# Performance work log

Hardware: AMD Instinct MI355X
Metric: run time of the kernel (lower is better)

Reference implementation:

```python
import jax, jax.numpy as jnp
import numpy as np

CHANNELS = 512
COND_DIM = 768
NUM_HEADS = 8
NUM_GROUPS = 32
EPS = 1e-5


def setup_inputs() -> dict:
    key = jax.random.key(0)
    ks = jax.random.split(key, 8)
    B, H, W, C, S = 8, 64, 64, CHANNELS, 256
    x = jax.random.normal(ks[0], (B, H, W, C), dtype=jnp.float32)
    cond_tokens = jax.random.normal(ks[1], (B, S, COND_DIM), dtype=jnp.float32)
    gn_scale = jnp.ones((C,), dtype=jnp.float32)
    gn_bias = jnp.zeros((C,), dtype=jnp.float32)
    Wq = jax.random.normal(ks[2], (C, CHANNELS), dtype=jnp.float32) * 0.02
    Wk = jax.random.normal(ks[3], (COND_DIM, CHANNELS), dtype=jnp.float32) * 0.02
    Wv = jax.random.normal(ks[4], (COND_DIM, CHANNELS), dtype=jnp.float32) * 0.02
    Wo = jax.random.normal(ks[5], (CHANNELS, CHANNELS), dtype=jnp.float32) * 0.02
    bo = jnp.zeros((CHANNELS,), dtype=jnp.float32)
    return {"x": x, "cond_tokens": cond_tokens, "gn_scale": gn_scale,
            "gn_bias": gn_bias, "Wq": Wq, "Wk": Wk, "Wv": Wv, "Wo": Wo, "bo": bo}


def group_norm(x, scale, bias):
    # x: (B,H,W,C); normalize over H,W and channels within each of NUM_GROUPS groups
    b, h, w, c = x.shape
    xg = x.reshape(b, h, w, NUM_GROUPS, c // NUM_GROUPS)
    mean = jnp.mean(xg, axis=(1, 2, 4), keepdims=True)
    var = jnp.var(xg, axis=(1, 2, 4), keepdims=True)
    xn = (xg - mean) * jax.lax.rsqrt(var + EPS)
    return xn.reshape(b, h, w, c) * scale + bias


def reference(x, cond_tokens, gn_scale, gn_bias, Wq, Wk, Wv, Wo, bo):
    b, h, w, c = x.shape
    head_dim = CHANNELS // NUM_HEADS
    x_seq = group_norm(x, gn_scale, gn_bias).reshape(b, h * w, c)
    # projections
    q = (x_seq @ Wq).reshape(b, -1, NUM_HEADS, head_dim).transpose(0, 2, 1, 3)
    k = (cond_tokens @ Wk).reshape(b, -1, NUM_HEADS, head_dim).transpose(0, 2, 1, 3)
    v = (cond_tokens @ Wv).reshape(b, -1, NUM_HEADS, head_dim).transpose(0, 2, 1, 3)
    scores = jnp.einsum('bhqd,bhkd->bhqk', q, k) / np.sqrt(head_dim).astype(np.float32)
    attn = jax.nn.softmax(scores, axis=-1)
    out = jnp.einsum('bhqk,bhkd->bhqd', attn, v)
    out = out.transpose(0, 2, 1, 3).reshape(b, h * w, CHANNELS)
    out = out @ Wo + bo
    return x + out.reshape(b, h, w, c)
```

## Files before the change

### kernel.cpp

```cpp
#include <hip/hip_runtime.h>
#include <hip/hip_bf16.h>

typedef unsigned short u16;
typedef unsigned int u32;
typedef __attribute__((ext_vector_type(8))) __bf16 bf16x8;
typedef __attribute__((ext_vector_type(4))) float f32x4;
typedef __attribute__((ext_vector_type(16))) float f32x16;
typedef __attribute__((ext_vector_type(4))) u32 u32x4;

#define DEVFN static __device__ __forceinline__

DEVFN float bf2f(u16 v) { union { u32 u; float f; } x; x.u = (u32)v << 16; return x.f; }
DEVFN u16 f2bf(float f) {
    union { float f; u32 u; } x; x.f = f;
    u32 r = x.u + 0x7fff + ((x.u >> 16) & 1);
    return (u16)(r >> 16);
}

union BF2 { struct { __bf16 lo, hi; } s; u32 w; };
DEVFN u32 pk2(float a, float b) { BF2 t; t.s.lo = (__bf16)a; t.s.hi = (__bf16)b; return t.w; }

DEVFN void gload_lds16(const u16* g, u16* l) {
    __builtin_amdgcn_global_load_lds((const __attribute__((address_space(1))) u32*)g,
                                     (__attribute__((address_space(3))) u32*)l, 16, 0, 0);
}

template<int OUTMODE, bool BIAS, bool RES, bool AFF>
__global__ __launch_bounds__(256)
void gemm_bt(const void* __restrict__ Av, const u16* __restrict__ B,
             void* __restrict__ Cv, const float* __restrict__ bias,
             const float* __restrict__ res,
             const float* __restrict__ cfA, const float* __restrict__ cfD,
             int K, int lda, int ldb, int ldc, float scale)
{
    __shared__ u16 smem[16384];
    const int tid = threadIdx.x;
    const int lane = tid & 63, wave = tid >> 6;
    const int wr = wave >> 1, wc = wave & 1;

    const u16* Bb = B + (long)blockIdx.y * 128 * ldb;
    const int foff = ((lane & 15) * 4 + (lane >> 4)) * 8;

    f32x4 acc[4][4];
#pragma unroll
    for (int i = 0; i < 4; ++i)
#pragma unroll
        for (int j = 0; j < 4; ++j) acc[i][j] = (f32x4){0.f, 0.f, 0.f, 0.f};

    for (int k0 = 0; k0 < K; k0 += 64) {
#pragma unroll
        for (int p = 0; p < 4; ++p) {
            int row = ((p & 1) * 4 + (tid >> 6)) * 16 + ((tid & 63) >> 2);
            int chl = (p >> 1) * 32 + (tid & 3) * 8;
            gload_lds16(Bb + (long)row * ldb + k0 + chl,
                        smem + 8192 + (p * 256 + tid) * 8);
        }
        if constexpr (AFF) {
            const float* xf = (const float*)Av;
#pragma unroll
            for (int p = 0; p < 4; ++p) {
                int row = ((p & 1) * 4 + (tid >> 6)) * 16 + ((tid & 63) >> 2);
                int chl = (p >> 1) * 32 + (tid & 3) * 8;
                long m = (long)blockIdx.x * 128 + row;
                int c = k0 + chl;
                const float* src = xf + m * lda + c;
                float4 v0 = *(const float4*)(src);
                float4 v1 = *(const float4*)(src + 4);
                int cb = (int)((m >> 12) << 9) + c;
                float4 a0 = *(const float4*)(cfA + cb);
                float4 a1 = *(const float4*)(cfA + cb + 4);
                float4 d0 = *(const float4*)(cfD + cb);
                float4 d1 = *(const float4*)(cfD + cb + 4);
                u32x4 o;
                o[0] = pk2(v0.x * a0.x + d0.x, v0.y * a0.y + d0.y);
                o[1] = pk2(v0.z * a0.z + d0.z, v0.w * a0.w + d0.w);
                o[2] = pk2(v1.x * a1.x + d1.x, v1.y * a1.y + d1.y);
                o[3] = pk2(v1.z * a1.z + d1.z, v1.w * a1.w + d1.w);
                *(u32x4*)(smem + (p * 256 + tid) * 8) = o;
            }
        } else {
            const u16* Ab = (const u16*)Av + (long)blockIdx.x * 128 * lda;
#pragma unroll
            for (int p = 0; p < 4; ++p) {
                int row = ((p & 1) * 4 + (tid >> 6)) * 16 + ((tid & 63) >> 2);
                int chl = (p >> 1) * 32 + (tid & 3) * 8;
                gload_lds16(Ab + (long)row * lda + k0 + chl,
                            smem + (p * 256 + tid) * 8);
            }
        }
        asm volatile("s_waitcnt vmcnt(0)" ::: "memory");
        __syncthreads();
#pragma unroll
        for (int kk = 0; kk < 2; ++kk) {
            bf16x8 av[4], bv[4];
#pragma unroll
            for (int i = 0; i < 4; ++i)
                av[i] = *(const bf16x8*)(smem + kk * 4096 + (wr * 4 + i) * 512 + foff);
#pragma unroll
            for (int j = 0; j < 4; ++j)
                bv[j] = *(const bf16x8*)(smem + 8192 + kk * 4096 + (wc * 4 + j) * 512 + foff);
#pragma unroll
            for (int i = 0; i < 4; ++i)
#pragma unroll
                for (int j = 0; j < 4; ++j)
                    acc[i][j] = __builtin_amdgcn_mfma_f32_16x16x32_bf16(av[i], bv[j], acc[i][j], 0, 0, 0);
        }
        __syncthreads();
    }

    const int m0 = blockIdx.x * 128 + wr * 64 + (lane >> 4) * 4;
    const int n0 = blockIdx.y * 128 + wc * 64 + (lane & 15);
    if constexpr (OUTMODE == 0) {
        u16* Cb = (u16*)Cv;
#pragma unroll
        for (int i = 0; i < 4; ++i)
#pragma unroll
            for (int j = 0; j < 4; ++j) {
                int n = n0 + j * 16;
#pragma unroll
                for (int r = 0; r < 4; ++r) {
                    int m = m0 + i * 16 + r;
                    Cb[(long)m * ldc + n] = f2bf(acc[i][j][r] * scale);
                }
            }
    } else if constexpr (OUTMODE == 1) {
        float* cl = (float*)smem;
        float* Co = (float*)Cv;
#pragma unroll
        for (int i = 0; i < 4; ++i) {
            __syncthreads();
#pragma unroll
            for (int j = 0; j < 4; ++j)
#pragma unroll
                for (int r = 0; r < 4; ++r) {
                    int rl = wr * 16 + (lane >> 4) * 4 + r;
                    int col = wc * 64 + j * 16 + (lane & 15);
                    cl[rl * 132 + col] = acc[i][j][r];
                }
            __syncthreads();
            int rl = tid >> 3;
            int c0 = (tid & 7) * 16;
            long m = (long)blockIdx.x * 128 + i * 16 + (rl & 15) + (rl >> 4) * 64;
            long n = (long)blockIdx.y * 128 + c0;
#pragma unroll
            for (int q = 0; q < 4; ++q) {
                float4 v = *(float4*)(cl + rl * 132 + c0 + q * 4);
                float4 o;
                o.x = v.x * scale; o.y = v.y * scale;
                o.z = v.z * scale; o.w = v.w * scale;
                if constexpr (BIAS) {
                    float4 b4 = *(const float4*)(bias + n + q * 4);
                    o.x += b4.x; o.y += b4.y; o.z += b4.z; o.w += b4.w;
                }
                if constexpr (RES) {
                    float4 r4 = *(const float4*)(res + m * ldc + n + q * 4);
                    o.x += r4.x; o.y += r4.y; o.z += r4.z; o.w += r4.w;
                }
                *(float4*)(Co + m * ldc + n + q * 4) = o;
            }
        }
    } else {
#pragma unroll
        for (int i = 0; i < 4; ++i) {
            int m = m0 + i * 16;
            int b = m >> 8, s = m & 255;
#pragma unroll
            for (int j = 0; j < 4; ++j) {
                int n = n0 + j * 16;
                int h = n >> 6, d = n & 63;
                ushort4 pk;
                pk.x = f2bf(acc[i][j][0]); pk.y = f2bf(acc[i][j][1]);
                pk.z = f2bf(acc[i][j][2]); pk.w = f2bf(acc[i][j][3]);
                *(ushort4*)((u16*)Cv + (((long)(b * 8 + h) * 64 + d) * 256 + s)) = pk;
            }
        }
    }
}

union U8 { u32 w[4]; bf16x8 v; };

__global__ __launch_bounds__(512, 4)
void attn_fused(const u16* __restrict__ Q, const u16* __restrict__ K,
                const u16* __restrict__ Vt, u16* __restrict__ O)
{
    __shared__ u16 lds[40960];
    const int tid = threadIdx.x, lane = tid & 63, wave = tid >> 6;
    const int bh = blockIdx.y, b = bh >> 3, h = bh & 7;
    const int l31 = lane & 31, lh = lane >> 5;
    const long q0 = (long)b * 4096 + blockIdx.x * 256 + wave * 32;
    const bool hiHalf = (lh != 0);

    {
        const u16* Kb_ = K + (long)b * 256 * 512 + h * 64;
        const u16* Vb_ = Vt + (long)bh * 16384;
#pragma unroll
        for (int it = 0; it < 4; ++it) {
            int f = it * 8 + wave;
            int st = f >> 2, kc = f & 3;
            gload_lds16(Kb_ + (long)(st * 32 + l31) * 512 + kc * 16 + lh * 8,
                        lds + f * 512 + lane * 8);
            int dt = f >> 4, ks = f & 15;
            gload_lds16(Vb_ + (long)(dt * 32 + l31) * 256 + ks * 16 + lh * 8,
                        lds + 16384 + f * 512 + lane * 8);
        }
    }
    bf16x8 qf[4];
    {
        const u16* Qp = Q + (q0 + l31) * 512 + h * 64 + lh * 8;
#pragma unroll
        for (int kc = 0; kc < 4; ++kc) qf[kc] = *(const bf16x8*)(Qp + kc * 16);
    }
    asm volatile("s_waitcnt vmcnt(0)" ::: "memory");
    __syncthreads();

    f32x16 oacc[2];
#pragma unroll
    for (int dt = 0; dt < 2; ++dt)
#pragma unroll
        for (int r = 0; r < 16; ++r) oacc[dt][r] = 0.f;
    float m_run = -3e38f, sum_run = 0.f;

#pragma unroll
    for (int st = 0; st < 8; ++st) {
        f32x16 sc;
#pragma unroll
        for (int r = 0; r < 16; ++r) sc[r] = 0.f;
        __builtin_amdgcn_s_setprio(1);
#pragma unroll
        for (int kc = 0; kc < 4; ++kc) {
            bf16x8 af = *(const bf16x8*)(lds + (st * 4 + kc) * 512 + lane * 8);
            sc = __builtin_amdgcn_mfma_f32_32x32x16_bf16(af, qf[kc], sc, 0, 0, 0);
        }
        __builtin_amdgcn_s_setprio(0);
        float tm = sc[0];
#pragma unroll
        for (int r = 1; r < 16; ++r) tm = fmaxf(tm, sc[r]);
        tm = fmaxf(tm, __shfl_xor(tm, 32));
        if (!__all(tm <= m_run + 8.f)) {
            float mnew = fmaxf(m_run, tm);
            float fac = exp2f(m_run - mnew);
            m_run = mnew;
            sum_run *= fac;
#pragma unroll
            for (int dt = 0; dt < 2; ++dt)
#pragma unroll
                for (int r = 0; r < 16; ++r) oacc[dt][r] *= fac;
        }
#pragma unroll
        for (int r = 0; r < 16; ++r) {
            float e = exp2f(sc[r] - m_run);
            sc[r] = e; sum_run += e;
        }
        u32 c[8], x[8];
#pragma unroll
        for (int i = 0; i < 8; ++i) c[i] = pk2(sc[2 * i], sc[2 * i + 1]);
#pragma unroll
        for (int i = 0; i < 8; ++i) x[i] = (u32)__shfl_xor((int)c[i], 32);
        U8 p0, p1;
        p0.w[0] = hiHalf ? x[2] : c[0];  p0.w[1] = hiHalf ? x[3] : c[1];
        p0.w[2] = hiHalf ? c[2] : x[0];  p0.w[3] = hiHalf ? c[3] : x[1];
        p1.w[0] = hiHalf ? x[6] : c[4];  p1.w[1] = hiHalf ? x[7] : c[5];
        p1.w[2] = hiHalf ? c[6] : x[4];  p1.w[3] = hiHalf ? c[7] : x[5];
        __builtin_amdgcn_s_setprio(1);
#pragma unroll
        for (int dt = 0; dt < 2; ++dt) {
            bf16x8 v0 = *(const bf16x8*)(lds + 16384 + (dt * 16 + st * 2) * 512 + lane * 8);
            bf16x8 v1 = *(const bf16x8*)(lds + 16384 + (dt * 16 + st * 2 + 1) * 512 + lane * 8);
            oacc[dt] = __builtin_amdgcn_mfma_f32_32x32x16_bf16(v0, p0.v, oacc[dt], 0, 0, 0);
            oacc[dt] = __builtin_amdgcn_mfma_f32_32x32x16_bf16(v1, p1.v, oacc[dt], 0, 0, 0);
        }
        __builtin_amdgcn_s_setprio(0);
    }

    sum_run += __shfl_xor(sum_run, 32);
    float inv = 1.f / sum_run;

    u16* ow = lds + 32768 + (wave & 3) * 2048;
    const int shift = wave >> 2;
#pragma unroll
    for (int s_ = 0; s_ < 2; ++s_) {
        if (s_ == 1) __syncthreads();
        if (shift == s_) {
            const int q = l31;
#pragma unroll
            for (int dt = 0; dt < 2; ++dt)
#pragma unroll
                for (int rq = 0; rq < 4; ++rq) {
                    int d = dt * 32 + rq * 8 + 4 * lh;
                    u32 w0 = pk2(oacc[dt][rq * 4 + 0] * inv, oacc[dt][rq * 4 + 1] * inv);
                    u32 w1 = pk2(oacc[dt][rq * 4 + 2] * inv, oacc[dt][rq * 4 + 3] * inv);
                    int byte = q * 128 + ((d * 2) ^ ((q & 7) << 4));
                    *(u32*)((char*)ow + byte) = w0;
                    *(u32*)((char*)ow + byte + 4) = w1;
                }
#pragma unroll
            for (int i = 0; i < 4; ++i) {
                int qq = (lane >> 3) + i * 8;
                int byte = qq * 128 + (((lane & 7) * 16) ^ ((qq & 7) << 4));
                bf16x8 val = *(const bf16x8*)((char*)ow + byte);
                *(bf16x8*)(O + (q0 + qq) * 512 + h * 64 + (lane & 7) * 8) = val;
            }
        }
    }
}

__global__ __launch_bounds__(256)
void gn_part(const float* __restrict__ x, float* __restrict__ part)
{
    const int b = blockIdx.x, ch = blockIdx.y;
    const float* base = x + ((long)b * 4096 + ch * 64) * 512;
    const int t = threadIdx.x;
    const int c4 = t & 127, r0 = t >> 7;
    float sum = 0.f, sq = 0.f;
    for (int rr = r0; rr < 64; rr += 2) {
        float4 v = *(const float4*)(base + (long)rr * 512 + c4 * 4);
        sum += v.x + v.y + v.z + v.w;
        sq  += v.x * v.x + v.y * v.y + v.z * v.z + v.w * v.w;
    }
    __shared__ float s0[128], s1[128];
    if (t >= 128) { s0[c4] = sum; s1[c4] = sq; }
    __syncthreads();
    if (t < 128) {
        sum += s0[c4]; sq += s1[c4];
        sum += __shfl_down(sum, 2); sum += __shfl_down(sum, 1);
        sq  += __shfl_down(sq, 2);  sq  += __shfl_down(sq, 1);
        if ((t & 3) == 0) {
            int g = t >> 2;
            float* pp = part + (long)(b * 64 + ch) * 64;
            pp[g] = sum; pp[32 + g] = sq;
        }
    }
}

__global__ __launch_bounds__(256)
void gn_coef(const float* __restrict__ part, const float* __restrict__ gscale,
             const float* __restrict__ gbias, float* __restrict__ coefA,
             float* __restrict__ coefD)
{
    const int t = threadIdx.x;
    const int b = t >> 5, g = t & 31;
    float S = 0.f, Q = 0.f;
    for (int ch = 0; ch < 64; ++ch) {
        const float* pp = part + (long)(b * 64 + ch) * 64;
        S += pp[g]; Q += pp[32 + g];
    }
    float mean = S * (1.f / 65536.f);
    float var = Q * (1.f / 65536.f) - mean * mean;
    float rstd = rsqrtf(var + 1e-5f);
#pragma unroll
    for (int cc = 0; cc < 16; ++cc) {
        int c = g * 16 + cc;
        float a = gscale[c] * rstd;
        coefA[b * 512 + c] = a;
        coefD[b * 512 + c] = gbias[c] - mean * a;
    }
}

__global__ __launch_bounds__(256)
void conv_bf16(const float* __restrict__ in, u16* __restrict__ out)
{
    long e = ((long)blockIdx.x * 256 + threadIdx.x) * 8;
    float4 v0 = *(const float4*)(in + e);
    float4 v1 = *(const float4*)(in + e + 4);
    float f[8] = { v0.x, v0.y, v0.z, v0.w, v1.x, v1.y, v1.z, v1.w };
    u32x4 o;
#pragma unroll
    for (int q = 0; q < 4; ++q)
        o[q] = (u32)f2bf(f[q * 2]) | ((u32)f2bf(f[q * 2 + 1]) << 16);
    *(u32x4*)(out + e) = o;
}

__global__ __launch_bounds__(256)
void transpose_all(const float* __restrict__ Wq, const float* __restrict__ Wk,
                   const float* __restrict__ Wv, const float* __restrict__ Wo,
                   u16* __restrict__ WqT, u16* __restrict__ WkT,
                   u16* __restrict__ WvT, u16* __restrict__ WoT)
{
    __shared__ u16 t[32][33];
    const int z = blockIdx.z;
    const float* in = (z == 0) ? Wq : (z == 1) ? Wk : (z == 2) ? Wv : Wo;
    u16* out = (z == 0) ? WqT : (z == 1) ? WkT : (z == 2) ? WvT : WoT;
    const int R = (z == 1 || z == 2) ? 768 : 512, C = 512;
    const int r0 = blockIdx.y * 32, c0 = blockIdx.x * 32;
    if (r0 >= R) return;
    int tx = threadIdx.x & 31, ty = threadIdx.x >> 5;
    for (int i = ty; i < 32; i += 8) t[i][tx] = f2bf(in[(long)(r0 + i) * C + c0 + tx]);
    __syncthreads();
    for (int i = ty; i < 32; i += 8) out[(long)(c0 + i) * R + r0 + tx] = t[tx][i];
}

extern "C" void kernel_launch(void* const* d_in, const int* in_sizes, int n_in,
                              void* d_out, int out_size, void* d_ws, size_t ws_size,
                              hipStream_t stream)
{
    const float* x    = (const float*)d_in[0];
    const float* cond = (const float*)d_in[1];
    const float* gsc  = (const float*)d_in[2];
    const float* gbi  = (const float*)d_in[3];
    const float* Wq   = (const float*)d_in[4];
    const float* Wk   = (const float*)d_in[5];
    const float* Wv   = (const float*)d_in[6];
    const float* Wo   = (const float*)d_in[7];
    const float* bo   = (const float*)d_in[8];

    char* ws = (char*)d_ws;
    size_t off = 0;
    auto alloc = [&](size_t bytes) -> void* {
        void* p = ws + off; off += (bytes + 255) & ~(size_t)255; return p;
    };
    u16* WqT    = (u16*)alloc(512 * 512 * 2);
    u16* WkT    = (u16*)alloc(512 * 768 * 2);
    u16* WvT    = (u16*)alloc(512 * 768 * 2);
    u16* WoT    = (u16*)alloc(512 * 512 * 2);
    float* cfA  = (float*)alloc(8 * 512 * 4);
    float* cfD  = (float*)alloc(8 * 512 * 4);
    float* part = (float*)alloc(8 * 64 * 64 * 4);
    u16* condb  = (u16*)alloc(2048l * 768 * 2);
    u16* Ob     = (u16*)alloc(33554432);
    u16* Qb     = (u16*)alloc(33554432);
    u16* Kb     = (u16*)alloc(2048l * 512 * 2);
    u16* Vt     = (u16*)alloc(2097152);

    transpose_all<<<dim3(16, 24, 4), 256, 0, stream>>>(Wq, Wk, Wv, Wo, WqT, WkT, WvT, WoT);
    conv_bf16<<<768, 256, 0, stream>>>(cond, condb);

    gn_part<<<dim3(8, 64), 256, 0, stream>>>(x, part);
    gn_coef<<<1, 256, 0, stream>>>(part, gsc, gbi, cfA, cfD);

    gemm_bt<0, false, false, true><<<dim3(256, 4), 256, 0, stream>>>(
        x, WqT, Qb, nullptr, nullptr, cfA, cfD, 512, 512, 512, 512,
        0.18033688011112042f);
    gemm_bt<0, false, false, false><<<dim3(16, 4), 256, 0, stream>>>(
        condb, WkT, Kb, nullptr, nullptr, nullptr, nullptr, 768, 768, 768, 512, 1.f);
    gemm_bt<2, false, false, false><<<dim3(16, 4), 256, 0, stream>>>(
        condb, WvT, Vt, nullptr, nullptr, nullptr, nullptr, 768, 768, 768, 0, 1.f);

    attn_fused<<<dim3(16, 64), 512, 0, stream>>>(Qb, Kb, Vt, Ob);

    gemm_bt<1, true, true, false><<<dim3(256, 4), 256, 0, stream>>>(
        Ob, WoT, d_out, bo, x, nullptr, nullptr, 512, 512, 512, 512, 1.f);
}
```

Before: 195.4 us.

## Double-buffer GEMM K-loop with prefetch and merge K/V projection launches

The GEMM main loop now uses a BK=32 double-buffered LDS pipeline. The next tile's global-to-LDS loads (or register-staged affine loads for the GroupNorm-fused Q projection) are issued before the MFMAs on the current tile, which removes one barrier per iteration and lets memory latency overlap compute. MFMA sections are wrapped in s_setprio. The separate K and V projection launches are merged into one grid with a z dimension that selects the weight and output layout. The cost is halved K per stage, which means more iterations and barriers, plus extra register pressure from the prefetched fp32 data.

Result: faster. 176.9 us (-9.4%).

```diff
diff --git a/kernel.cpp b/kernel.cpp
--- a/kernel.cpp
+++ b/kernel.cpp
@@ -28,8 +28,9 @@
 template<int OUTMODE, bool BIAS, bool RES, bool AFF>
 __global__ __launch_bounds__(256)
 void gemm_bt(const void* __restrict__ Av, const u16* __restrict__ B,
-             void* __restrict__ Cv, const float* __restrict__ bias,
-             const float* __restrict__ res,
+             const u16* __restrict__ B2,
+             void* __restrict__ Cv, void* __restrict__ Cv2,
+             const float* __restrict__ bias, const float* __restrict__ res,
              const float* __restrict__ cfA, const float* __restrict__ cfD,
              int K, int lda, int ldb, int ldc, float scale)
 {
@@ -37,8 +38,9 @@
     const int tid = threadIdx.x;
     const int lane = tid & 63, wave = tid >> 6;
     const int wr = wave >> 1, wc = wave & 1;
-
-    const u16* Bb = B + (long)blockIdx.y * 128 * ldb;
+    const u16* Bsel = (OUTMODE == 3 && blockIdx.z) ? B2 : B;
+    const u16* Bb = Bsel + (long)blockIdx.y * 128 * ldb;
+    const int ra = tid >> 2, ca = (tid & 3) * 8;
     const int foff = ((lane & 15) * 4 + (lane >> 4)) * 8;
 
     f32x4 acc[4][4];
@@ -47,65 +49,87 @@
 #pragma unroll
         for (int j = 0; j < 4; ++j) acc[i][j] = (f32x4){0.f, 0.f, 0.f, 0.f};
 
-    for (int k0 = 0; k0 < K; k0 += 64) {
-#pragma unroll
-        for (int p = 0; p < 4; ++p) {
-            int row = ((p & 1) * 4 + (tid >> 6)) * 16 + ((tid & 63) >> 2);
-            int chl = (p >> 1) * 32 + (tid & 3) * 8;
-            gload_lds16(Bb + (long)row * ldb + k0 + chl,
-                        smem + 8192 + (p * 256 + tid) * 8);
-        }
-        if constexpr (AFF) {
-            const float* xf = (const float*)Av;
-#pragma unroll
-            for (int p = 0; p < 4; ++p) {
-                int row = ((p & 1) * 4 + (tid >> 6)) * 16 + ((tid & 63) >> 2);
-                int chl = (p >> 1) * 32 + (tid & 3) * 8;
-                long m = (long)blockIdx.x * 128 + row;
-                int c = k0 + chl;
-                const float* src = xf + m * lda + c;
-                float4 v0 = *(const float4*)(src);
-                float4 v1 = *(const float4*)(src + 4);
-                int cb = (int)((m >> 12) << 9) + c;
-                float4 a0 = *(const float4*)(cfA + cb);
-                float4 a1 = *(const float4*)(cfA + cb + 4);
-                float4 d0 = *(const float4*)(cfD + cb);
-                float4 d1 = *(const float4*)(cfD + cb + 4);
-                u32x4 o;
-                o[0] = pk2(v0.x * a0.x + d0.x, v0.y * a0.y + d0.y);
-                o[1] = pk2(v0.z * a0.z + d0.z, v0.w * a0.w + d0.w);
-                o[2] = pk2(v1.x * a1.x + d1.x, v1.y * a1.y + d1.y);
-                o[3] = pk2(v1.z * a1.z + d1.z, v1.w * a1.w + d1.w);
-                *(u32x4*)(smem + (p * 256 + tid) * 8) = o;
-            }
-        } else {
-            const u16* Ab = (const u16*)Av + (long)blockIdx.x * 128 * lda;
-#pragma unroll
-            for (int p = 0; p < 4; ++p) {
-                int row = ((p & 1) * 4 + (tid >> 6)) * 16 + ((tid & 63) >> 2);
-                int chl = (p >> 1) * 32 + (tid & 3) * 8;
-                gload_lds16(Ab + (long)row * lda + k0 + chl,
-                            smem + (p * 256 + tid) * 8);
-            }
-        }
+    const int nt = K >> 5;
+
+    auto stageB = [&](int t, u16* bb) {
+#pragma unroll
+        for (int p = 0; p < 2; ++p)
+            gload_lds16(Bb + (long)(p * 64 + ra) * ldb + t * 32 + ca,
+                        bb + (p * 256 + tid) * 8);
+    };
+    const u16* Ab = (const u16*)Av + (long)blockIdx.x * 128 * lda;
+    auto stageA = [&](int t, u16* ab) {
+#pragma unroll
+        for (int p = 0; p < 2; ++p)
+            gload_lds16(Ab + (long)(p * 64 + ra) * lda + t * 32 + ca,
+                        ab + (p * 256 + tid) * 8);
+    };
+    const float* xf = (const float*)Av;
+    float4 xr[2][2], ar[2][2], dr[2][2];
+    auto affLoad = [&](int t) {
+#pragma unroll
+        for (int p = 0; p < 2; ++p) {
+            long m = (long)blockIdx.x * 128 + p * 64 + ra;
+            int c = t * 32 + ca;
+            const float* src = xf + m * lda + c;
+            xr[p][0] = *(const float4*)(src);
+            xr[p][1] = *(const float4*)(src + 4);
+            int cb = (int)((m >> 12) << 9) + c;
+            ar[p][0] = *(const float4*)(cfA + cb);
+            ar[p][1] = *(const float4*)(cfA + cb + 4);
+            dr[p][0] = *(const float4*)(cfD + cb);
+            dr[p][1] = *(const float4*)(cfD + cb + 4);
+        }
+    };
+    auto affWrite = [&](u16* ab) {
+#pragma unroll
+        for (int p = 0; p < 2; ++p) {
+            u32x4 o;
+            o[0] = pk2(xr[p][0].x * ar[p][0].x + dr[p][0].x,
+                       xr[p][0].y * ar[p][0].y + dr[p][0].y);
+            o[1] = pk2(xr[p][0].z * ar[p][0].z + dr[p][0].z,
+                       xr[p][0].w * ar[p][0].w + dr[p][0].w);
+            o[2] = pk2(xr[p][1].x * ar[p][1].x + dr[p][1].x,
+                       xr[p][1].y * ar[p][1].y + dr[p][1].y);
+            o[3] = pk2(xr[p][1].z * ar[p][1].z + dr[p][1].z,
+                       xr[p][1].w * ar[p][1].w + dr[p][1].w);
+            *(u32x4*)(ab + (p * 256 + tid) * 8) = o;
+        }
+    };
+
+    stageB(0, smem + 4096);
+    if constexpr (AFF) { affLoad(0); affWrite(smem); }
+    else               stageA(0, smem);
+
+    int cur = 0;
+    for (int t = 0; t < nt; ++t) {
         asm volatile("s_waitcnt vmcnt(0)" ::: "memory");
         __syncthreads();
-#pragma unroll
-        for (int kk = 0; kk < 2; ++kk) {
-            bf16x8 av[4], bv[4];
-#pragma unroll
-            for (int i = 0; i < 4; ++i)
-                av[i] = *(const bf16x8*)(smem + kk * 4096 + (wr * 4 + i) * 512 + foff);
+        const int nxt = cur ^ 1;
+        u16* cA = smem + cur * 8192;
+        u16* cB = smem + cur * 8192 + 4096;
+        u16* nA = smem + nxt * 8192;
+        u16* nB = smem + nxt * 8192 + 4096;
+        const bool more = (t + 1 < nt);
+        if (more) {
+            stageB(t + 1, nB);
+            if constexpr (AFF) affLoad(t + 1);
+            else               stageA(t + 1, nA);
+        }
+        bf16x8 av[4], bv[4];
+#pragma unroll
+        for (int i = 0; i < 4; ++i) av[i] = *(const bf16x8*)(cA + (wr * 4 + i) * 512 + foff);
+#pragma unroll
+        for (int j = 0; j < 4; ++j) bv[j] = *(const bf16x8*)(cB + (wc * 4 + j) * 512 + foff);
+        __builtin_amdgcn_s_setprio(1);
+#pragma unroll
+        for (int i = 0; i < 4; ++i)
 #pragma unroll
             for (int j = 0; j < 4; ++j)
-                bv[j] = *(const bf16x8*)(smem + 8192 + kk * 4096 + (wc * 4 + j) * 512 + foff);
-#pragma unroll
-            for (int i = 0; i < 4; ++i)
-#pragma unroll
-                for (int j = 0; j < 4; ++j)
-                    acc[i][j] = __builtin_amdgcn_mfma_f32_16x16x32_bf16(av[i], bv[j], acc[i][j], 0, 0, 0);
-        }
-        __syncthreads();
+                acc[i][j] = __builtin_amdgcn_mfma_f32_16x16x32_bf16(av[i], bv[j], acc[i][j], 0, 0, 0);
+        __builtin_amdgcn_s_setprio(0);
+        if (more) { if constexpr (AFF) affWrite(nA); }
+        cur = nxt;
     }
 
     const int m0 = blockIdx.x * 128 + wr * 64 + (lane >> 4) * 4;
@@ -159,7 +183,7 @@
                 *(float4*)(Co + m * ldc + n + q * 4) = o;
             }
         }
-    } else {
+    } else if constexpr (OUTMODE == 2) {
 #pragma unroll
         for (int i = 0; i < 4; ++i) {
             int m = m0 + i * 16;
@@ -172,6 +196,36 @@
                 pk.x = f2bf(acc[i][j][0]); pk.y = f2bf(acc[i][j][1]);
                 pk.z = f2bf(acc[i][j][2]); pk.w = f2bf(acc[i][j][3]);
                 *(ushort4*)((u16*)Cv + (((long)(b * 8 + h) * 64 + d) * 256 + s)) = pk;
+            }
+        }
+    } else {
+        if (blockIdx.z == 0) {
+            u16* Cb = (u16*)Cv;
+#pragma unroll
+            for (int i = 0; i < 4; ++i)
+#pragma unroll
+                for (int j = 0; j < 4; ++j) {
+                    int n = n0 + j * 16;
+#pragma unroll
+                    for (int r = 0; r < 4; ++r) {
+                        int m = m0 + i * 16 + r;
+                        Cb[(long)m * ldc + n] = f2bf(acc[i][j][r] * scale);
+                    }
+                }
+        } else {
+#pragma unroll
+            for (int i = 0; i < 4; ++i) {
+                int m = m0 + i * 16;
+                int b = m >> 8, s = m & 255;
+#pragma unroll
+                for (int j = 0; j < 4; ++j) {
+                    int n = n0 + j * 16;
+                    int h = n >> 6, d = n & 63;
+                    ushort4 pk;
+                    pk.x = f2bf(acc[i][j][0]); pk.y = f2bf(acc[i][j][1]);
+                    pk.z = f2bf(acc[i][j][2]); pk.w = f2bf(acc[i][j][3]);
+                    *(ushort4*)((u16*)Cv2 + (((long)(b * 8 + h) * 64 + d) * 256 + s)) = pk;
+                }
             }
         }
     }
@@ -428,15 +482,15 @@
     gn_coef<<<1, 256, 0, stream>>>(part, gsc, gbi, cfA, cfD);
 
     gemm_bt<0, false, false, true><<<dim3(256, 4), 256, 0, stream>>>(
-        x, WqT, Qb, nullptr, nullptr, cfA, cfD, 512, 512, 512, 512,
-        0.18033688011112042f);
-    gemm_bt<0, false, false, false><<<dim3(16, 4), 256, 0, stream>>>(
-        condb, WkT, Kb, nullptr, nullptr, nullptr, nullptr, 768, 768, 768, 512, 1.f);
-    gemm_bt<2, false, false, false><<<dim3(16, 4), 256, 0, stream>>>(
-        condb, WvT, Vt, nullptr, nullptr, nullptr, nullptr, 768, 768, 768, 0, 1.f);
+        x, WqT, nullptr, Qb, nullptr, nullptr, nullptr, cfA, cfD,
+        512, 512, 512, 512, 0.18033688011112042f);
+    gemm_bt<3, false, false, false><<<dim3(16, 4, 2), 256, 0, stream>>>(
+        condb, WkT, WvT, Kb, Vt, nullptr, nullptr, nullptr, nullptr,
+        768, 768, 768, 512, 1.f);
 
     attn_fused<<<dim3(16, 64), 512, 0, stream>>>(Qb, Kb, Vt, Ob);
 
     gemm_bt<1, true, true, false><<<dim3(256, 4), 256, 0, stream>>>(
-        Ob, WoT, d_out, bo, x, nullptr, nullptr, 512, 512, 512, 512, 1.f);
-}
+        Ob, WoT, nullptr, d_out, nullptr, bo, x, nullptr, nullptr,
+        512, 512, 512, 512, 1.f);
+}
```
